# Kernel tuning notes

Measured on AMD Instinct MI355X. Metric: run time of the kernel, lower is better.

The kernel has to match this reference:

```python
import jax, jax.numpy as jnp
import numpy as np

# --- spiking logic gates expressed as exact float {0,1} algebra ---
def XOR(a, b):  return a + b - 2.0 * a * b
def AND(a, b):  return a * b
def OR(a, b):   return a + b - a * b
def NOT(a):     return 1.0 - a
def MUX(s, a, b):  # s==1 -> a, s==0 -> b (matches MUXGate usage in source)
    return s * a + (1.0 - s) * b

def adder_bits(A, B):
    """Ripple-carry adder, MSB at index 0 (Adder12Bit)."""
    n = A.shape[-1]
    carry = jnp.zeros_like(A[..., 0:1])
    outs = [None] * n
    for i in range(n - 1, -1, -1):
        a, b = A[..., i:i + 1], B[..., i:i + 1]
        t1 = XOR(a, b)
        outs[i] = XOR(t1, carry)
        carry = OR(OR(AND(a, b), AND(a, carry)), AND(b, carry))
    return jnp.concatenate(outs, -1), carry

def subtract_bits(A, B):
    """Ripple-borrow subtractor A-B, MSB at index 0 (Subtractor12Bit/4Bit)."""
    n = A.shape[-1]
    borrow = jnp.zeros_like(A[..., 0:1])
    outs = [None] * n
    for i in range(n - 1, -1, -1):
        a, b = A[..., i:i + 1], B[..., i:i + 1]
        axb = XOR(a, b)
        outs[i] = XOR(axb, borrow)
        borrow = OR(AND(NOT(a), b), AND(NOT(axb), borrow))
    return jnp.concatenate(outs, -1), borrow

def comparator4(A, B):
    """Comparator4Bit: A,B [...,4] MSB first -> (a_gt_b, a_eq_b)."""
    eq = NOT(XOR(A, B))
    gt = AND(A, NOT(B))
    eq3, eq2, eq1, eq0 = (eq[..., i:i + 1] for i in range(4))
    gt3, gt2, gt1, gt0 = (gt[..., i:i + 1] for i in range(4))
    eq32 = AND(eq3, eq2)
    eq321 = AND(eq32, eq1)
    a_gt_b = OR(OR(OR(gt3, AND(eq3, gt2)), AND(eq32, gt1)), AND(eq321, gt0))
    a_eq_b = AND(eq321, eq0)
    return a_gt_b, a_eq_b

def barrel_right12(X, shift):
    """BarrelShifterRight12: X [...,12], shift [...,4] MSB first."""
    z = jnp.zeros_like(X[..., 0:1])
    s0, s1, s2, s3 = shift[..., 3:4], shift[..., 2:3], shift[..., 1:2], shift[..., 0:1]
    x = MUX(s0, jnp.concatenate([z, X[..., :11]], -1), X)          # >>1
    x = MUX(s1, jnp.concatenate([z, z, x[..., :10]], -1), x)       # >>2
    x = MUX(s2, jnp.concatenate([z] * 4 + [x[..., :8]], -1), x)    # >>4
    x = MUX(s3, jnp.concatenate([z] * 8 + [x[..., :4]], -1), x)    # >>8
    return x

def barrel_left8(X, shift):
    """BarrelShifterLeft8: X [...,8], shift [...,3] MSB first."""
    z = jnp.zeros_like(X[..., 0:1])
    s0, s1, s2 = shift[..., 2:3], shift[..., 1:2], shift[..., 0:1]
    x = MUX(s0, jnp.concatenate([X[..., 1:], z], -1), X)            # <<1
    x = MUX(s1, jnp.concatenate([x[..., 2:], z, z], -1), x)         # <<2
    x = MUX(s2, jnp.concatenate([x[..., 4:]] + [z] * 4, -1), x)     # <<4
    return x

def lzd8(X):
    """LeadingZeroDetector8: X [...,8] MSB at index 0 -> [...,3] lz count."""
    b7, b6, b5, b4 = X[..., 0:1], X[..., 1:2], X[..., 2:3], X[..., 3:4]
    b3, b2, b1, b0 = X[..., 4:5], X[..., 5:6], X[..., 6:7], X[..., 7:8]
    has76, has54 = OR(b7, b6), OR(b5, b4)
    has32, has10 = OR(b3, b2), OR(b1, b0)
    has7654 = OR(has76, has54)
    lzc2 = NOT(has7654)
    lzc1 = MUX(has7654, NOT(has76), NOT(has32))
    lzc0_high = MUX(has76, NOT(b7), NOT(b5))
    lzc0_low = MUX(has32, NOT(b3), NOT(b1))
    lzc0 = MUX(has7654, lzc0_high, lzc0_low)
    return jnp.concatenate([lzc2, lzc1, lzc0], -1)

def increment4(A):
    """4-bit +1 incrementer (half-adder ripple), MSB first."""
    carry = jnp.ones_like(A[..., 0:1])
    outs = [None] * 4
    for i in range(3, -1, -1):
        a = A[..., i:i + 1]
        outs[i] = XOR(a, carry)
        carry = AND(a, carry)
    return jnp.concatenate(outs, -1)

def fp8_add(A, B):
    """SpikeFP8Adder_Spatial: E4M3 bit vectors [...,8] (sign|exp4|man3, MSB first)."""
    sa, ea, ma = A[..., 0:1], A[..., 1:5], A[..., 5:8]
    sb, eb, mb = B[..., 0:1], B[..., 1:5], B[..., 5:8]
    # 1) exponent comparison & operand swap (larger exponent -> L)
    a_gt_b, a_eq_b = comparator4(ea, eb)
    sel = OR(a_gt_b, a_eq_b)                      # pick A when exp_a >= exp_b
    exp_l, exp_s = MUX(sel, ea, eb), MUX(sel, eb, ea)
    man_l, man_s = MUX(sel, ma, mb), MUX(sel, mb, ma)
    sign_l, sign_s = MUX(sel, sa, sb), MUX(sel, sb, sa)
    # 2) exponent difference (4-bit) for alignment
    diff4, _ = subtract_bits(exp_l, exp_s)
    # 3) extended 12-bit mantissas: [ovf, hidden, m2,m1,m0, 7 guard zeros]
    hid_l = OR(OR(exp_l[..., 0:1], exp_l[..., 1:2]), OR(exp_l[..., 2:3], exp_l[..., 3:4]))
    hid_s = OR(OR(exp_s[..., 0:1], exp_s[..., 1:2]), OR(exp_s[..., 2:3], exp_s[..., 3:4]))
    z = jnp.zeros_like(sa)
    ext_l = jnp.concatenate([z, hid_l, man_l] + [z] * 7, -1)
    ext_s = jnp.concatenate([z, hid_s, man_s] + [z] * 7, -1)
    ext_s = barrel_right12(ext_s, diff4)
    # 4) add when signs equal, subtract when they differ
    same_sign = NOT(XOR(sign_l, sign_s))
    ssum, _ = adder_bits(ext_l, ext_s)
    sdif, _ = subtract_bits(ext_l, ext_s)
    mant = MUX(same_sign, ssum, sdif)             # [...,12]
    # 5) normalize using top 8 bits: LZD + barrel left shift
    top8 = mant[..., 0:8]
    lzc = lzd8(top8)                              # [...,3]
    norm = barrel_left8(top8, lzc)
    # 6) exponent adjust: exp_new = exp_l - lzc + 1
    lzc4 = jnp.concatenate([z, lzc], -1)
    exp_sub, _ = subtract_bits(exp_l, lzc4)
    exp_new = increment4(exp_sub)
    # 7) pack result: sign | exp4 | mantissa (bits 1..3 after hidden bit)
    return jnp.concatenate([sign_l, exp_new, norm[..., 1:4]], -1)

def setup_inputs() -> dict:
    key = jax.random.key(0)
    kA, kB = jax.random.split(key)
    N = 4_194_304
    A = jax.random.bernoulli(kA, 0.5, (N, 8)).astype(jnp.float32)
    B = jax.random.bernoulli(kB, 0.5, (N, 8)).astype(jnp.float32)
    return {"A": A, "B": B}

def reference(A, B):
    return fp8_add(A, B)
```

## Files before the change

kernel.cpp:

```cpp
#include <hip/hip_runtime.h>


typedef unsigned int uint32x4 __attribute__((ext_vector_type(4)));

__device__ __forceinline__ unsigned bit_of(unsigned u) { return (u >> 23) & 1u; }
__device__ __forceinline__ unsigned f_of(unsigned b)   { return b ? 0x3F800000u : 0u; }

__device__ __forceinline__ void fp8_add_row(const uint32x4& a0, const uint32x4& a1,
                                            const uint32x4& b0, const uint32x4& b1,
                                            uint32x4& o0, uint32x4& o1)
{
    unsigned sa = bit_of(a0.x);
    unsigned ea = (bit_of(a0.y) << 3) | (bit_of(a0.z) << 2) | (bit_of(a0.w) << 1) | bit_of(a1.x);
    unsigned ma = (bit_of(a1.y) << 2) | (bit_of(a1.z) << 1) | bit_of(a1.w);
    unsigned sb = bit_of(b0.x);
    unsigned eb = (bit_of(b0.y) << 3) | (bit_of(b0.z) << 2) | (bit_of(b0.w) << 1) | bit_of(b1.x);
    unsigned mb = (bit_of(b1.y) << 2) | (bit_of(b1.z) << 1) | bit_of(b1.w);

    unsigned sel = (ea >= eb) ? 1u : 0u;
    unsigned exp_l = sel ? ea : eb, exp_s = sel ? eb : ea;
    unsigned man_l = sel ? ma : mb, man_s = sel ? mb : ma;
    unsigned sign_l = sel ? sa : sb, sign_s = sel ? sb : sa;

    unsigned diff = (exp_l - exp_s) & 0xFu;
    unsigned hid_l = exp_l ? 1u : 0u;
    unsigned hid_s = exp_s ? 1u : 0u;

    unsigned ext_l = (hid_l << 10) | (man_l << 7);
    unsigned ext_s = ((hid_s << 10) | (man_s << 7)) >> diff;

    unsigned same_sign = (sign_l == sign_s);
    unsigned mant = same_sign ? ((ext_l + ext_s) & 0xFFFu)
                              : ((ext_l - ext_s) & 0xFFFu);

    unsigned top8 = mant >> 4;
    unsigned lzc = top8 ? (unsigned)(__clz((int)top8) - 24) : 7u;
    unsigned norm = (top8 << lzc) & 0xFFu;

    unsigned exp_new = (exp_l - lzc + 1u) & 0xFu;
    unsigned man_out = (norm >> 4) & 0x7u;

    o0.x = f_of(sign_l);
    o0.y = f_of((exp_new >> 3) & 1u);
    o0.z = f_of((exp_new >> 2) & 1u);
    o0.w = f_of((exp_new >> 1) & 1u);
    o1.x = f_of(exp_new & 1u);
    o1.y = f_of((man_out >> 2) & 1u);
    o1.z = f_of((man_out >> 1) & 1u);
    o1.w = f_of(man_out & 1u);
}

constexpr int RPT = 4;
constexpr int BLOCK = 256;
constexpr int ROWS_PER_BLOCK = BLOCK * RPT;

__global__ __launch_bounds__(BLOCK) void fp8_adder_fast(
    const uint32x4* __restrict__ A, const uint32x4* __restrict__ B,
    uint32x4* __restrict__ O)
{
    int base = blockIdx.x * ROWS_PER_BLOCK + threadIdx.x;

    uint32x4 a0[RPT], a1[RPT], b0[RPT], b1[RPT];
    #pragma unroll
    for (int k = 0; k < RPT; ++k) {
        int i = base + k * BLOCK;
        a0[k] = __builtin_nontemporal_load(&A[2 * i]);
        a1[k] = __builtin_nontemporal_load(&A[2 * i + 1]);
        b0[k] = __builtin_nontemporal_load(&B[2 * i]);
        b1[k] = __builtin_nontemporal_load(&B[2 * i + 1]);
    }

    #pragma unroll
    for (int k = 0; k < RPT; ++k) {
        int i = base + k * BLOCK;
        uint32x4 o0, o1;
        fp8_add_row(a0[k], a1[k], b0[k], b1[k], o0, o1);
        __builtin_nontemporal_store(o0, &O[2 * i]);
        __builtin_nontemporal_store(o1, &O[2 * i + 1]);
    }
}

__global__ __launch_bounds__(BLOCK) void fp8_adder_tail(
    const uint32x4* __restrict__ A, const uint32x4* __restrict__ B,
    uint32x4* __restrict__ O, int row0, int n_rows)
{
    int i = row0 + blockIdx.x * BLOCK + threadIdx.x;
    if (i >= n_rows) return;
    uint32x4 a0 = __builtin_nontemporal_load(&A[2 * i]);
    uint32x4 a1 = __builtin_nontemporal_load(&A[2 * i + 1]);
    uint32x4 b0 = __builtin_nontemporal_load(&B[2 * i]);
    uint32x4 b1 = __builtin_nontemporal_load(&B[2 * i + 1]);
    uint32x4 o0, o1;
    fp8_add_row(a0, a1, b0, b1, o0, o1);
    __builtin_nontemporal_store(o0, &O[2 * i]);
    __builtin_nontemporal_store(o1, &O[2 * i + 1]);
}

extern "C" void kernel_launch(void* const* d_in, const int* in_sizes, int n_in,
                              void* d_out, int out_size, void* d_ws, size_t ws_size,
                              hipStream_t stream) {
    const uint32x4* A = (const uint32x4*)d_in[0];
    const uint32x4* B = (const uint32x4*)d_in[1];
    uint32x4* O = (uint32x4*)d_out;
    int n_rows = in_sizes[0] / 8;

    int full_blocks = n_rows / ROWS_PER_BLOCK;
    int done_rows = full_blocks * ROWS_PER_BLOCK;
    int rem = n_rows - done_rows;

    if (full_blocks > 0)
        fp8_adder_fast<<<full_blocks, BLOCK, 0, stream>>>(A, B, O);
    if (rem > 0) {
        int tail_blocks = (rem + BLOCK - 1) / BLOCK;
        fp8_adder_tail<<<tail_blocks, BLOCK, 0, stream>>>(A, B, O, done_rows, n_rows);
    }
}
```

Measured before the change: 299.8 us.

## Stage row loads and stores through swizzled LDS for fully contiguous wave access

Each wave now loads a contiguous chunk of A and B, one 16-byte vector per lane, so every global instruction covers a dense 1 KiB span. The vectors are then transposed through XOR-swizzled shared memory so each lane gets its own row's two halves. Outputs go back through LDS the same way and are written contiguously. This adds LDS traffic and per-iteration write-read dependencies with no explicit barrier, relying on wave-synchronous execution. It also drops the loop that issued all loads up front, which reduces memory-level parallelism.

```diff
diff --git a/kernel.cpp b/kernel.cpp
--- a/kernel.cpp
+++ b/kernel.cpp
@@ -5,6 +5,8 @@
 
 __device__ __forceinline__ unsigned bit_of(unsigned u) { return (u >> 23) & 1u; }
 __device__ __forceinline__ unsigned f_of(unsigned b)   { return b ? 0x3F800000u : 0u; }
+
+__device__ __forceinline__ int swz(int m) { return m ^ ((m >> 3) & 7); }
 
 __device__ __forceinline__ void fp8_add_row(const uint32x4& a0, const uint32x4& a1,
                                             const uint32x4& b0, const uint32x4& b1,
@@ -52,31 +54,50 @@
 
 constexpr int RPT = 4;
 constexpr int BLOCK = 256;
+constexpr int WAVES = BLOCK / 64;
 constexpr int ROWS_PER_BLOCK = BLOCK * RPT;
 
 __global__ __launch_bounds__(BLOCK) void fp8_adder_fast(
     const uint32x4* __restrict__ A, const uint32x4* __restrict__ B,
     uint32x4* __restrict__ O)
 {
-    int base = blockIdx.x * ROWS_PER_BLOCK + threadIdx.x;
+    __shared__ uint32x4 sh[WAVES * 256];
 
-    uint32x4 a0[RPT], a1[RPT], b0[RPT], b1[RPT];
-    #pragma unroll
-    for (int k = 0; k < RPT; ++k) {
-        int i = base + k * BLOCK;
-        a0[k] = __builtin_nontemporal_load(&A[2 * i]);
-        a1[k] = __builtin_nontemporal_load(&A[2 * i + 1]);
-        b0[k] = __builtin_nontemporal_load(&B[2 * i]);
-        b1[k] = __builtin_nontemporal_load(&B[2 * i + 1]);
-    }
+    int lane = threadIdx.x & 63;
+    int w = threadIdx.x >> 6;
+    uint32x4* shW = &sh[w * 256];
+
+    int rowBase = blockIdx.x * ROWS_PER_BLOCK + w * (64 * RPT);
 
     #pragma unroll
     for (int k = 0; k < RPT; ++k) {
-        int i = base + k * BLOCK;
+        int WW = 2 * (rowBase + k * 64);
+
+        uint32x4 vA0 = __builtin_nontemporal_load(&A[WW + lane]);
+        uint32x4 vA1 = __builtin_nontemporal_load(&A[WW + 64 + lane]);
+        uint32x4 vB0 = __builtin_nontemporal_load(&B[WW + lane]);
+        uint32x4 vB1 = __builtin_nontemporal_load(&B[WW + 64 + lane]);
+
+        shW[swz(lane)]            = vA0;
+        shW[swz(64 + lane)]       = vA1;
+        shW[128 + swz(lane)]      = vB0;
+        shW[128 + swz(64 + lane)] = vB1;
+
+        uint32x4 a0 = shW[swz(2 * lane)];
+        uint32x4 a1 = shW[swz(2 * lane + 1)];
+        uint32x4 b0 = shW[128 + swz(2 * lane)];
+        uint32x4 b1 = shW[128 + swz(2 * lane + 1)];
+
         uint32x4 o0, o1;
-        fp8_add_row(a0[k], a1[k], b0[k], b1[k], o0, o1);
-        __builtin_nontemporal_store(o0, &O[2 * i]);
-        __builtin_nontemporal_store(o1, &O[2 * i + 1]);
+        fp8_add_row(a0, a1, b0, b1, o0, o1);
+
+        shW[swz(2 * lane)]     = o0;
+        shW[swz(2 * lane + 1)] = o1;
+
+        uint32x4 w0 = shW[swz(lane)];
+        uint32x4 w1 = shW[swz(64 + lane)];
+        __builtin_nontemporal_store(w0, &O[WW + lane]);
+        __builtin_nontemporal_store(w1, &O[WW + 64 + lane]);
     }
 }
 
```

Measured after the change: 293.6 us. 1.02x faster.
